# Performance work log

Measured on AMD Instinct MI355X. Metric: run time of the kernel, lower is better.

The kernel has to match this reference:

```python
import jax, jax.numpy as jnp
import numpy as np

B, S, D, H, T = 16, 512, 512, 8, 8
DK = D // H
SCALE = float(1.0 / np.sqrt(DK))
EPS = 1e-5


def setup_inputs() -> dict:
    key = jax.random.key(0)
    ks = jax.random.split(key, 12)
    s = float(1.0 / np.sqrt(D))  # torch Linear default init scale
    u = lambda k, shp: jax.random.uniform(k, shp, jnp.float32, -s, s)
    return {
        "x": jax.random.normal(ks[0], (B, S, D), jnp.float32),
        "x_type": jax.random.randint(ks[1], (B, S), 0, T, jnp.int32),
        "mask": jax.random.randint(ks[2], (B, S, S), 0, 2, jnp.int32),
        "Wq": u(ks[3], (T, D, D)), "bq": u(ks[4], (T, D)),
        "Wk": u(ks[5], (T, D, D)), "bk": u(ks[6], (T, D)),
        "Wv": u(ks[7], (T, D, D)), "bv": u(ks[8], (T, D)),
        "Wa": u(ks[9], (T, D, D)), "ba": u(ks[10], (T, D)),
        "gamma": jnp.ones((T, D), jnp.float32),
        "beta": jnp.zeros((T, D), jnp.float32),
    }


def _typed_proj(xf, t, W, b):
    # per-node-type linear 'experts': compute all T projections, select by type id
    # xf: [N, D], W: [T, D, D], b: [T, D], t: [N] -> [N, D]
    all_p = jnp.einsum('nd,tdh->nth', xf, W) + b[None]  # [N, T, D]
    return jnp.take_along_axis(all_p, t[:, None, None], axis=1)[:, 0]


def reference(x, x_type, mask, Wq, bq, Wk, bk, Wv, bv, Wa, ba, gamma, beta):
    xf = x.reshape(-1, D)          # [N, D], N = B*S
    t = x_type.reshape(-1)         # [N]

    # heterogeneous Q/K/V dispatch
    q = _typed_proj(xf, t, Wq, bq).reshape(B, S, H, DK).transpose(0, 2, 1, 3)
    k = _typed_proj(xf, t, Wk, bk).reshape(B, S, H, DK).transpose(0, 2, 1, 3)
    v = _typed_proj(xf, t, Wv, bv).reshape(B, S, H, DK).transpose(0, 2, 1, 3)

    # scaled dot-product attention with boolean mask (mask==0 -> -1e9)
    scores = jnp.einsum('bhqd,bhkd->bhqk', q, k) * SCALE  # [B, H, S, S]
    scores = jnp.where(mask[:, None] == 0, jnp.float32(-1e9), scores)
    p = jax.nn.softmax(scores, axis=-1)
    att = jnp.einsum('bhqk,bhkd->bhqd', p, v)             # [B, H, S, DK]
    att = att.transpose(0, 2, 1, 3).reshape(-1, D)        # [N, D]

    # per-type output projection + residual + per-type LayerNorm
    a = _typed_proj(att, t, Wa, ba)
    h = a + xf
    mu = jnp.mean(h, axis=-1, keepdims=True)
    var = jnp.mean((h - mu) ** 2, axis=-1, keepdims=True)
    out = (h - mu) * jax.lax.rsqrt(var + EPS) * gamma[t] + beta[t]
    return out.reshape(B, S, D)
```

## Files before the change

kernel.cpp:

```cpp
#include <hip/hip_runtime.h>
#include <hip/hip_bf16.h>

typedef __attribute__((ext_vector_type(8))) short short8;
typedef __attribute__((ext_vector_type(4))) float f32x4;
typedef __attribute__((ext_vector_type(4))) unsigned short u16x4;
typedef unsigned short u16;
typedef unsigned int u32;
typedef unsigned long long u64;

#define NB 16
#define NS 512
#define ND 512
#define NH 8
#define NT 8
#define NDK 64
#define NN (NB*NS)
#define SCALE_LOG2E 0.18033688011112042f
#define BM 128
#define BN 128
#define BKK 64

__device__ __forceinline__ u16 f2bf(float f) {
    __hip_bfloat16 h = __float2bfloat16(f);
    return *reinterpret_cast<u16*>(&h);
}
__device__ __forceinline__ float bf2f(u16 b) {
    u32 u = ((u32)b) << 16;
    return *reinterpret_cast<float*>(&u);
}
__device__ __forceinline__ u32 pk2(float lo, float hi) {
    return (u32)f2bf(lo) | ((u32)f2bf(hi) << 16);
}

typedef const __attribute__((address_space(1))) void* gas_t;
typedef __attribute__((address_space(3))) void* las_t;

__device__ __forceinline__ void gload16(const void* gsrc, void* ldst) {
    __builtin_amdgcn_global_load_lds((gas_t)gsrc, (las_t)ldst, 16, 0, 0);
}

__global__ __launch_bounds__(256) void pre_all(
    const float* __restrict__ x, const int* __restrict__ xty, const int* __restrict__ mask,
    const float* __restrict__ Wq, const float* __restrict__ Wk,
    const float* __restrict__ Wv, const float* __restrict__ Wa,
    u16* __restrict__ xb,
    u16* __restrict__ Wqt, u16* __restrict__ Wkt, u16* __restrict__ Wvt, u16* __restrict__ Wat,
    u64* __restrict__ maskb, int* __restrict__ scnt)
{
    __shared__ __align__(16) float tile[64][68];
    __shared__ int cnt[NT];
    int bid = blockIdx.x, tid = threadIdx.x;

    if (bid < 4096) {
        int i = bid * 256 + tid;
        float4 v = reinterpret_cast<const float4*>(x)[i];
        u16x4 o;
        o.x = f2bf(v.x); o.y = f2bf(v.y); o.z = f2bf(v.z); o.w = f2bf(v.w);
        reinterpret_cast<u16x4*>(xb)[i] = o;
    } else if (bid < 6144) {
        int wid = bid - 4096;
        int bx = wid & 7, by = (wid >> 3) & 7, bz = wid >> 6;
        int arr = bz >> 3, t = bz & 7;
        const float* W = (arr == 0 ? Wq : arr == 1 ? Wk : arr == 2 ? Wv : Wa) + ((size_t)t << 18);
        u16* O = (arr == 0 ? Wqt : arr == 1 ? Wkt : arr == 2 ? Wvt : Wat) + ((size_t)t << 18);
        int d0 = bx * 64, h0 = by * 64;
        int tx = tid & 15, ty = tid >> 4;
        #pragma unroll
        for (int i = 0; i < 4; ++i) {
            int r = ty + i * 16;
            float4 v = *reinterpret_cast<const float4*>(&W[(size_t)(d0 + r) * ND + h0 + tx * 4]);
            *reinterpret_cast<float4*>(&tile[r][tx * 4]) = v;
        }
        __syncthreads();
        #pragma unroll
        for (int i = 0; i < 4; ++i) {
            int r = ty + i * 16;
            u16x4 o;
            o.x = f2bf(tile[tx * 4 + 0][r]);
            o.y = f2bf(tile[tx * 4 + 1][r]);
            o.z = f2bf(tile[tx * 4 + 2][r]);
            o.w = f2bf(tile[tx * 4 + 3][r]);
            *reinterpret_cast<u16x4*>(&O[(size_t)(h0 + r) * ND + d0 + tx * 4]) = o;
        }
    } else if (bid < 7168) {
        int base = (bid - 6144) * 16;
        #pragma unroll
        for (int c = 0; c < 16; ++c) {
            int i = (base + c) * 256 + tid;
            int v = mask[i];
            u64 bal = __ballot(v != 0);
            if ((tid & 63) == 0) maskb[i >> 6] = bal;
        }
    } else {
        int s = bid - 7168;
        if (tid < NT) cnt[tid] = 0;
        __syncthreads();
        if (tid < 128) atomicAdd(&cnt[xty[s * 128 + tid]], 1);
        __syncthreads();
        if (tid < NT) scnt[s * 8 + tid] = cnt[tid];
    }
}

__global__ __launch_bounds__(256) void scatter_k(
    const int* __restrict__ xty, const int* __restrict__ scnt,
    int* __restrict__ perm, int* __restrict__ typeoff,
    int* __restrict__ tile_type, int* __restrict__ tile_row0, int* __restrict__ ntiles)
{
    __shared__ int base[NT], tot[NT];
    int s = blockIdx.x, tid = threadIdx.x;
    if (tid < NT) {
        int tt = 0;
        for (int ss = 0; ss < 64; ++ss) tt += scnt[ss * 8 + tid];
        tot[tid] = tt;
    }
    __syncthreads();
    if (tid < NT) {
        int off = 0;
        for (int u = 0; u < tid; ++u) off += tot[u];
        base[tid] = off;
    }
    __syncthreads();
    {
        int t = tid & 7;
        for (int ss = tid >> 3; ss < s; ss += 32) atomicAdd(&base[t], scnt[ss * 8 + t]);
    }
    __syncthreads();
    if (tid < 128) {
        int n = s * 128 + tid;
        int t = xty[n];
        int p = atomicAdd(&base[t], 1);
        perm[p] = n;
    }
    if (s == 0 && tid == 0) {
        int acc = 0, nt = 0;
        for (int t = 0; t < NT; ++t) {
            typeoff[t] = acc;
            int c = tot[t];
            for (int r = 0; r < c; r += BM) { tile_type[nt] = t; tile_row0[nt] = acc + r; ++nt; }
            acc += c;
        }
        typeoff[NT] = acc;
        *ntiles = nt;
    }
}

__global__ __launch_bounds__(256) void qkv_gemm(
    const u16* __restrict__ xb,
    const u16* __restrict__ Wqt, const u16* __restrict__ Wkt, const u16* __restrict__ Wvt,
    const float* __restrict__ bq, const float* __restrict__ bk, const float* __restrict__ bv,
    const int* __restrict__ perm, const int* __restrict__ typeoff,
    const int* __restrict__ tile_type, const int* __restrict__ tile_row0, const int* __restrict__ ntiles,
    u16* __restrict__ qb, u16* __restrict__ kbf, u16* __restrict__ vb)
{
    int p = (blockIdx.x & 7) * 54 + (blockIdx.x >> 3);
    int tile = p / 6;
    if (tile >= *ntiles) return;
    int pairc = p % 6;
    int proj = pairc >> 1;
    int colbase = (pairc & 1) * 256;
    int t = tile_type[tile];
    int row0 = tile_row0[tile];
    int rows = typeoff[t + 1] - row0; if (rows > BM) rows = BM;
    const u16* W = (proj == 0 ? Wqt : proj == 1 ? Wkt : Wvt) + ((size_t)t << 18);
    const float* bias = (proj == 0 ? bq : proj == 1 ? bk : bv) + (t << 9);
    u16* outp = proj == 0 ? qb : proj == 1 ? kbf : vb;
    float qscale = proj == 0 ? SCALE_LOG2E : 1.f;

    __shared__ __align__(16) u16 smem[2][2][BM][BKK];
    __shared__ int stok[BM];

    int tid = threadIdx.x;
    if (tid < BM) stok[tid] = perm[row0 + (tid < rows ? tid : 0)];
    __syncthreads();

    int lane = tid & 63, w = tid >> 6;
    int wr = w >> 1, wc = w & 1;
    int fr = lane & 15, g = lane >> 4;
    int lrow = lane >> 3;
    int schunk = (lane & 7) ^ lrow;
    int tokA[4];
    #pragma unroll
    for (int k = 0; k < 4; ++k) tokA[k] = stok[w * 32 + k * 8 + lrow];

    auto stage = [&](int buf, int k0, int c0) {
        #pragma unroll
        for (int k = 0; k < 4; ++k) {
            gload16(xb + (((size_t)tokA[k]) << 9) + k0 + schunk * 8, &smem[buf][0][w * 32 + k * 8][0]);
            gload16(W + (((size_t)(c0 + w * 32 + k * 8 + lrow)) << 9) + k0 + schunk * 8,
                    &smem[buf][1][w * 32 + k * 8][0]);
        }
    };

    f32x4 acc[4][4] = {};

    auto epilogue = [&](int buf, int c0) {
        u16* sT = &smem[buf][0][0][0];
        #pragma unroll
        for (int n = 0; n < 4; ++n) {
            int wcol = wc * 64 + n * 16 + fr;
            float bv_ = bias[c0 + wcol];
            #pragma unroll
            for (int m = 0; m < 4; ++m)
                #pragma unroll
                for (int i = 0; i < 4; ++i) {
                    int r = wr * 64 + m * 16 + g * 4 + i;
                    int ch = (wcol >> 3) ^ (r & 7);
                    sT[r * 128 + ch * 8 + (wcol & 7)] = f2bf((acc[m][n][i] + bv_) * qscale);
                }
        }
        asm volatile("s_waitcnt lgkmcnt(0)" ::: "memory");
        __builtin_amdgcn_s_barrier();
        int r = tid >> 1, h2 = tid & 1;
        if (r < rows) {
            int tok = stok[r], b = tok >> 9, s = tok & 511;
            int h = (c0 >> 6) + h2;
            u16* dst = outp + ((size_t)((b * NH + h) * NS + s) << 6);
            #pragma unroll
            for (int j2 = 0; j2 < 8; ++j2) {
                int ch = (h2 * 8 + j2) ^ (r & 7);
                *reinterpret_cast<short8*>(dst + j2 * 8) =
                    *reinterpret_cast<const short8*>(&sT[r * 128 + ch * 8]);
            }
        }
        asm volatile("s_waitcnt lgkmcnt(0)" ::: "memory");
        __builtin_amdgcn_s_barrier();
        #pragma unroll
        for (int m = 0; m < 4; ++m)
            #pragma unroll
            for (int n = 0; n < 4; ++n)
                acc[m][n] = (f32x4){0.f, 0.f, 0.f, 0.f};
    };

    stage(0, 0, colbase);
    #pragma unroll
    for (int j = 0; j < 16; ++j) {
        int cur = j & 1;
        if (j < 15) {
            int jn = j + 1;
            stage(cur ^ 1, (jn & 7) * BKK, colbase + (jn >> 3) * BN);
            asm volatile("s_waitcnt vmcnt(8)" ::: "memory");
        } else {
            asm volatile("s_waitcnt vmcnt(0)" ::: "memory");
        }
        __builtin_amdgcn_s_barrier();

        const char* Ab = (const char*)&smem[cur][0][0][0];
        const char* Bb = (const char*)&smem[cur][1][0][0];
        #pragma unroll
        for (int ks = 0; ks < 2; ++ks) {
            short8 af[4], bfr[4];
            #pragma unroll
            for (int m = 0; m < 4; ++m) {
                int r = wr * 64 + m * 16 + fr;
                af[m] = *reinterpret_cast<const short8*>(Ab + r * 128 + (((ks * 4 + g) ^ (r & 7)) << 4));
            }
            #pragma unroll
            for (int n = 0; n < 4; ++n) {
                int r = wc * 64 + n * 16 + fr;
                bfr[n] = *reinterpret_cast<const short8*>(Bb + r * 128 + (((ks * 4 + g) ^ (r & 7)) << 4));
            }
            #pragma unroll
            for (int m = 0; m < 4; ++m)
                #pragma unroll
                for (int n = 0; n < 4; ++n)
                    acc[m][n] = __builtin_amdgcn_mfma_f32_16x16x32_bf16(af[m], bfr[n], acc[m][n], 0, 0, 0);
        }
        asm volatile("s_waitcnt lgkmcnt(0)" ::: "memory");
        __builtin_amdgcn_s_barrier();

        if (j == 7) epilogue(1, colbase);
    }
    epilogue(1, colbase + BN);
}

__global__ __launch_bounds__(256) void transp_v(const u16* __restrict__ vb, u16* __restrict__ vtb)
{
    int bh = blockIdx.y, s0 = blockIdx.x * 64;
    __shared__ __align__(16) u16 t[64][72];
    int tid = threadIdx.x;
    const u16* src = vb + ((size_t)bh << 15) + ((size_t)s0 << 6);
    #pragma unroll
    for (int it = 0; it < 2; ++it) {
        int idx = it * 256 + tid;
        int s = idx & 63, c = idx >> 6;
        short8 v = *reinterpret_cast<const short8*>(src + ((size_t)s << 6) + c * 8);
        #pragma unroll
        for (int j = 0; j < 8; ++j) t[c * 8 + j][s] = ((const u16*)&v)[j];
    }
    __syncthreads();
    u16* dst = vtb + ((size_t)bh << 15) + s0;
    #pragma unroll
    for (int it = 0; it < 2; ++it) {
        int idx = it * 256 + tid;
        int dk = idx >> 3, c = idx & 7;
        short8 v = *reinterpret_cast<const short8*>(&t[dk][c * 8]);
        *reinterpret_cast<short8*>(dst + (size_t)dk * NS + c * 8) = v;
    }
}

__global__ __launch_bounds__(256) void attn_mfma(
    const u16* __restrict__ qb, const u16* __restrict__ kbf, const u16* __restrict__ vtb,
    const u64* __restrict__ maskb, u16* __restrict__ attb)
{
    int work = (blockIdx.x & 7) * 128 + (blockIdx.x >> 3);
    int bh = work >> 3, jq = work & 7;
    int b = bh >> 3, h = bh & 7;
    int q0 = jq * 64;
    int tid = threadIdx.x, lane = tid & 63, w = tid >> 6;
    int ln15 = lane & 15, g = lane >> 4;

    __shared__ __align__(16) u16 sK[64 * 64];
    __shared__ __align__(16) u16 sVt[64 * 64];
    __shared__ __align__(16) u16 sP[4 * 16 * 68];

    const u16* Qg = qb + ((size_t)(bh * NS + q0 + w * 16 + ln15) << 6);
    short8 aq0 = *reinterpret_cast<const short8*>(Qg + g * 8);
    short8 aq1 = *reinterpret_cast<const short8*>(Qg + 32 + g * 8);

    const u16* Kg = kbf + ((size_t)bh << 15);
    const u16* Vtg = vtb + ((size_t)bh << 15);
    int srow = tid >> 3, schunk = tid & 7;

    const u64* Mq = maskb + ((size_t)((b << 9) + q0 + w * 16 + ln15)) * 8;
    float mrun = -3.0e38f, lrun = 0.f;
    f32x4 acc_o[4] = {};

    short8 kpre0 = *reinterpret_cast<const short8*>(Kg + ((size_t)srow << 6) + schunk * 8);
    short8 kpre1 = *reinterpret_cast<const short8*>(Kg + ((size_t)(srow + 32) << 6) + schunk * 8);
    short8 vpre0 = *reinterpret_cast<const short8*>(Vtg + (size_t)srow * NS + schunk * 8);
    short8 vpre1 = *reinterpret_cast<const short8*>(Vtg + (size_t)(srow + 32) * NS + schunk * 8);

    char* sPw = (char*)sP + w * 16 * 136;

    for (int j = 0; j < 8; ++j) {
        __syncthreads();
        {
            int r2 = srow + 32;
            *reinterpret_cast<short8*>((char*)sK  + srow * 128 + ((schunk * 16) ^ ((srow & 7) << 4))) = kpre0;
            *reinterpret_cast<short8*>((char*)sK  + r2   * 128 + ((schunk * 16) ^ ((r2   & 7) << 4))) = kpre1;
            *reinterpret_cast<short8*>((char*)sVt + srow * 128 + ((schunk * 16) ^ ((srow & 7) << 4))) = vpre0;
            *reinterpret_cast<short8*>((char*)sVt + r2   * 128 + ((schunk * 16) ^ ((r2   & 7) << 4))) = vpre1;
        }
        if (j < 7) {
            int j1 = j + 1;
            kpre0 = *reinterpret_cast<const short8*>(Kg + ((size_t)(j1 * 64 + srow) << 6) + schunk * 8);
            kpre1 = *reinterpret_cast<const short8*>(Kg + ((size_t)(j1 * 64 + srow + 32) << 6) + schunk * 8);
            vpre0 = *reinterpret_cast<const short8*>(Vtg + (size_t)srow * NS + j1 * 64 + schunk * 8);
            vpre1 = *reinterpret_cast<const short8*>(Vtg + (size_t)(srow + 32) * NS + j1 * 64 + schunk * 8);
        }
        __syncthreads();

        f32x4 accs[4] = {};
        __builtin_amdgcn_s_setprio(1);
        #pragma unroll
        for (int ks = 0; ks < 2; ++ks) {
            short8 bq_ = ks ? aq1 : aq0;
            #pragma unroll
            for (int n = 0; n < 4; ++n) {
                int row = n * 16 + ln15;
                short8 kfrag = *reinterpret_cast<const short8*>(
                    (char*)sK + row * 128 + (((ks * 64) + g * 16) ^ ((row & 7) << 4)));
                accs[n] = __builtin_amdgcn_mfma_f32_16x16x32_bf16(kfrag, bq_, accs[n], 0, 0, 0);
            }
        }
        __builtin_amdgcn_s_setprio(0);

        u64 mw = Mq[j];
        float sv[4][4];
        float mx = -3.0e38f;
        #pragma unroll
        for (int n = 0; n < 4; ++n) {
            u32 b4 = (u32)(mw >> (n * 16 + g * 4)) & 15u;
            #pragma unroll
            for (int r = 0; r < 4; ++r) {
                float s = (b4 >> r) & 1u ? accs[n][r] : -1.0e9f;
                sv[n][r] = s;
                mx = fmaxf(mx, s);
            }
        }
        mx = fmaxf(mx, __shfl_xor(mx, 16));
        mx = fmaxf(mx, __shfl_xor(mx, 32));

        if (__any(mx > mrun + 8.f)) {
            float nm = fmaxf(mrun, mx);
            float sc = exp2f(mrun - nm);
            mrun = nm;
            lrun *= sc;
            #pragma unroll
            for (int i = 0; i < 4; ++i) {
                float si = __shfl(sc, g * 4 + i);
                #pragma unroll
                for (int n2 = 0; n2 < 4; ++n2) acc_o[n2][i] *= si;
            }
        }

        float ps = 0.f;
        #pragma unroll
        for (int n = 0; n < 4; ++n) {
            float p0 = exp2f(sv[n][0] - mrun), p1 = exp2f(sv[n][1] - mrun);
            float p2 = exp2f(sv[n][2] - mrun), p3 = exp2f(sv[n][3] - mrun);
            ps += (p0 + p1) + (p2 + p3);
            *reinterpret_cast<u32*>(sPw + ln15 * 136 + n * 32 + g * 8 + 0) = pk2(p0, p1);
            *reinterpret_cast<u32*>(sPw + ln15 * 136 + n * 32 + g * 8 + 4) = pk2(p2, p3);
        }
        ps += __shfl_xor(ps, 16);
        ps += __shfl_xor(ps, 32);
        lrun += ps;

        __builtin_amdgcn_s_setprio(1);
        #pragma unroll
        for (int ks = 0; ks < 2; ++ks) {
            short8 ap = *reinterpret_cast<const short8*>(sPw + ln15 * 136 + ks * 64 + g * 16);
            #pragma unroll
            for (int n2 = 0; n2 < 4; ++n2) {
                int row = n2 * 16 + ln15;
                short8 vfrag = *reinterpret_cast<const short8*>(
                    (char*)sVt + row * 128 + (((ks * 64) + g * 16) ^ ((row & 7) << 4)));
                acc_o[n2] = __builtin_amdgcn_mfma_f32_16x16x32_bf16(ap, vfrag, acc_o[n2], 0, 0, 0);
            }
        }
        __builtin_amdgcn_s_setprio(0);
    }

    float linv = 1.f / lrun;
    #pragma unroll
    for (int i = 0; i < 4; ++i) {
        float li = __shfl(linv, g * 4 + i);
        int q = q0 + w * 16 + g * 4 + i;
        #pragma unroll
        for (int n2 = 0; n2 < 4; ++n2) {
            attb[((size_t)((b << 9) + q) << 9) + (h << 6) + n2 * 16 + ln15] =
                f2bf(acc_o[n2][i] * li);
        }
    }
}

__global__ __launch_bounds__(256) void out_gemm(
    const u16* __restrict__ attb, const u16* __restrict__ Wat, const float* __restrict__ ba,
    const int* __restrict__ perm, const int* __restrict__ typeoff,
    const int* __restrict__ tile_type, const int* __restrict__ tile_row0, const int* __restrict__ ntiles,
    const u16* __restrict__ xb, u16* __restrict__ hbuf)
{
    int work = (blockIdx.x & 7) * 36 + (blockIdx.x >> 3);
    int tile = work >> 2;
    if (tile >= *ntiles) return;
    int t = tile_type[tile];
    int row0 = tile_row0[tile];
    int rows = typeoff[t + 1] - row0; if (rows > BM) rows = BM;
    int col0 = (work & 3) * BN;
    const u16* W = Wat + ((size_t)t << 18);
    const float* bias = ba + (t << 9);

    __shared__ __align__(16) u16 As[2][BM][BKK];
    __shared__ __align__(16) u16 Bs[2][BM][BKK];
    __shared__ int stok[BM];

    int tid = threadIdx.x;
    if (tid < BM) stok[tid] = perm[row0 + (tid < rows ? tid : 0)];
    __syncthreads();

    int lane = tid & 63, w = tid >> 6;
    int wr = w >> 1, wc = w & 1;
    int fr = lane & 15, g = lane >> 4;

    int lrow = lane >> 3;
    int schunk = (lane & 7) ^ lrow;
    int tokA[4];
    #pragma unroll
    for (int k = 0; k < 4; ++k) tokA[k] = stok[w * 32 + k * 8 + lrow];

    auto stage = [&](int buf, int k0) {
        #pragma unroll
        for (int k = 0; k < 4; ++k) {
            gload16(attb + (((size_t)tokA[k]) << 9) + k0 + schunk * 8, &As[buf][w * 32 + k * 8][0]);
            gload16(W + (((size_t)(col0 + w * 32 + k * 8 + lrow)) << 9) + k0 + schunk * 8,
                    &Bs[buf][w * 32 + k * 8][0]);
        }
    };

    f32x4 acc[4][4] = {};

    stage(0, 0);
    #pragma unroll
    for (int it = 0; it < 8; ++it) {
        int cur = it & 1;
        if (it < 7) {
            stage(cur ^ 1, (it + 1) * BKK);
            asm volatile("s_waitcnt vmcnt(8)" ::: "memory");
        } else {
            asm volatile("s_waitcnt vmcnt(0)" ::: "memory");
        }
        __builtin_amdgcn_s_barrier();

        const char* Ab = (const char*)As[cur];
        const char* Bb = (const char*)Bs[cur];
        #pragma unroll
        for (int ks = 0; ks < 2; ++ks) {
            short8 af[4], bfr[4];
            #pragma unroll
            for (int m = 0; m < 4; ++m) {
                int r = wr * 64 + m * 16 + fr;
                af[m] = *reinterpret_cast<const short8*>(Ab + r * 128 + (((ks * 4 + g) ^ (r & 7)) << 4));
            }
            #pragma unroll
            for (int n = 0; n < 4; ++n) {
                int r = wc * 64 + n * 16 + fr;
                bfr[n] = *reinterpret_cast<const short8*>(Bb + r * 128 + (((ks * 4 + g) ^ (r & 7)) << 4));
            }
            #pragma unroll
            for (int m = 0; m < 4; ++m)
                #pragma unroll
                for (int n = 0; n < 4; ++n)
                    acc[m][n] = __builtin_amdgcn_mfma_f32_16x16x32_bf16(af[m], bfr[n], acc[m][n], 0, 0, 0);
        }
        asm volatile("s_waitcnt lgkmcnt(0)" ::: "memory");
        __builtin_amdgcn_s_barrier();
    }

    int rbase = g << 2;
    #pragma unroll
    for (int n = 0; n < 4; ++n) {
        int c = col0 + wc * 64 + n * 16 + fr;
        float bv_ = bias[c];
        #pragma unroll
        for (int m = 0; m < 4; ++m) {
            #pragma unroll
            for (int i = 0; i < 4; ++i) {
                int r = wr * 64 + m * 16 + rbase + i;
                if (r < rows) {
                    int tok = stok[r];
                    size_t off = (size_t)tok * ND + c;
                    hbuf[off] = f2bf(acc[m][n][i] + bv_ + bf2f(xb[off]));
                }
            }
        }
    }
}

__global__ __launch_bounds__(256) void lnorm(
    const u16* __restrict__ hbuf, const int* __restrict__ xty,
    const float* __restrict__ gamma, const float* __restrict__ beta, float* __restrict__ out)
{
    int row = blockIdx.x * 4 + (threadIdx.x >> 6);
    int lane = threadIdx.x & 63;
    short8 v = *reinterpret_cast<const short8*>(hbuf + (size_t)row * ND + lane * 8);
    float f[8];
    float sum = 0.f, sq = 0.f;
    #pragma unroll
    for (int k = 0; k < 8; ++k) {
        f[k] = bf2f(((const u16*)&v)[k]);
        sum += f[k];
        sq += f[k] * f[k];
    }
    #pragma unroll
    for (int off = 32; off; off >>= 1) { sum += __shfl_xor(sum, off); sq += __shfl_xor(sq, off); }
    float mu = sum * (1.f / ND);
    float var = sq * (1.f / ND) - mu * mu;
    float is = rsqrtf(var + 1e-5f);
    int t = xty[row];
    const float4* g4 = reinterpret_cast<const float4*>(gamma + ((size_t)t << 9) + lane * 8);
    const float4* b4 = reinterpret_cast<const float4*>(beta + ((size_t)t << 9) + lane * 8);
    float4 g0 = g4[0], g1 = g4[1];
    float4 b0 = b4[0], b1 = b4[1];
    float4 o0, o1;
    o0.x = (f[0] - mu) * is * g0.x + b0.x;
    o0.y = (f[1] - mu) * is * g0.y + b0.y;
    o0.z = (f[2] - mu) * is * g0.z + b0.z;
    o0.w = (f[3] - mu) * is * g0.w + b0.w;
    o1.x = (f[4] - mu) * is * g1.x + b1.x;
    o1.y = (f[5] - mu) * is * g1.y + b1.y;
    o1.z = (f[6] - mu) * is * g1.z + b1.z;
    o1.w = (f[7] - mu) * is * g1.w + b1.w;
    float4* out4 = reinterpret_cast<float4*>(out + (size_t)row * ND + lane * 8);
    out4[0] = o0; out4[1] = o1;
}

extern "C" void kernel_launch(void* const* d_in, const int* in_sizes, int n_in,
                              void* d_out, int out_size, void* d_ws, size_t ws_size,
                              hipStream_t stream)
{
    const float* x     = (const float*)d_in[0];
    const int*   xty   = (const int*)d_in[1];
    const int*   mask  = (const int*)d_in[2];
    const float* Wq    = (const float*)d_in[3];
    const float* bq    = (const float*)d_in[4];
    const float* Wk    = (const float*)d_in[5];
    const float* bk    = (const float*)d_in[6];
    const float* Wv    = (const float*)d_in[7];
    const float* bv    = (const float*)d_in[8];
    const float* Wa    = (const float*)d_in[9];
    const float* ba    = (const float*)d_in[10];
    const float* gamma = (const float*)d_in[11];
    const float* beta  = (const float*)d_in[12];
    float* out = (float*)d_out;

    char* ws = (char*)d_ws;
    u16*   xb      = (u16*)(ws + 0);
    u16*   Wqt     = (u16*)(ws + 8388608);
    u16*   Wkt     = (u16*)(ws + 12582912);
    u16*   Wvt     = (u16*)(ws + 16777216);
    u16*   Wat     = (u16*)(ws + 20971520);
    u16*   qb      = (u16*)(ws + 25165824);
    u16*   kbf     = (u16*)(ws + 33554432);
    u16*   vb      = (u16*)(ws + 41943040);
    u16*   vtb     = (u16*)(ws + 50331648);
    u16*   attb    = (u16*)(ws + 58720256);
    u16*   hbuf    = (u16*)(ws + 67108864);
    u64*   maskb   = (u64*)(ws + 83886080);
    int*   perm    = (int*)(ws + 84410368);
    int*   typeoff = (int*)(ws + 84443136);
    int*   ttile   = (int*)(ws + 84443200);
    int*   trow    = (int*)(ws + 84443776);
    int*   ntiles  = (int*)(ws + 84444352);
    int*   scnt    = (int*)(ws + 84444480);

    pre_all<<<dim3(7232), dim3(256), 0, stream>>>(x, xty, mask, Wq, Wk, Wv, Wa,
                                                  xb, Wqt, Wkt, Wvt, Wat, maskb, scnt);
    scatter_k<<<dim3(64), dim3(256), 0, stream>>>(xty, scnt, perm, typeoff, ttile, trow, ntiles);
    qkv_gemm<<<dim3(432), dim3(256), 0, stream>>>(xb, Wqt, Wkt, Wvt, bq, bk, bv,
                                                  perm, typeoff, ttile, trow, ntiles, qb, kbf, vb);
    transp_v<<<dim3(8, 128), dim3(256), 0, stream>>>(vb, vtb);
    attn_mfma<<<dim3(1024), dim3(256), 0, stream>>>(qb, kbf, vtb, maskb, attb);
    out_gemm<<<dim3(288), dim3(256), 0, stream>>>(attb, Wat, ba,
                                                  perm, typeoff, ttile, trow, ntiles, xb, hbuf);
    lnorm<<<dim3(2048), dim3(256), 0, stream>>>(hbuf, xty, gamma, beta, out);
}
```

Measured before the change: 251.2 us.

## Split QKV GEMM to one column tile per block and keep P in registers

The QKV GEMM now assigns one 128-column tile per block instead of two, which doubles the grid and removes the mid-loop epilogue. The epilogue uses a padded unswizzled staging array. In attention, the softmax probabilities are packed straight into MFMA operand registers instead of going through a shared-memory sP buffer. The V tile stores into LDS are permuted with 4-element writes to match that register layout. The change trades the A-tile reuse across column tiles for more parallelism, and it relies on the new V permutation matching the implicit P fragment order.

```diff
diff --git a/kernel.cpp b/kernel.cpp
--- a/kernel.cpp
+++ b/kernel.cpp
@@ -152,15 +152,14 @@
     const int* __restrict__ tile_type, const int* __restrict__ tile_row0, const int* __restrict__ ntiles,
     u16* __restrict__ qb, u16* __restrict__ kbf, u16* __restrict__ vb)
 {
-    int p = (blockIdx.x & 7) * 54 + (blockIdx.x >> 3);
-    int tile = p / 6;
+    int work = (blockIdx.x & 7) * 108 + (blockIdx.x >> 3);
+    int tile = work / 12, pc = work % 12;
     if (tile >= *ntiles) return;
-    int pairc = p % 6;
-    int proj = pairc >> 1;
-    int colbase = (pairc & 1) * 256;
     int t = tile_type[tile];
     int row0 = tile_row0[tile];
     int rows = typeoff[t + 1] - row0; if (rows > BM) rows = BM;
+    int proj = pc >> 2;
+    int col0 = (pc & 3) * BN;
     const u16* W = (proj == 0 ? Wqt : proj == 1 ? Wkt : Wvt) + ((size_t)t << 18);
     const float* bias = (proj == 0 ? bq : proj == 1 ? bk : bv) + (t << 9);
     u16* outp = proj == 0 ? qb : proj == 1 ? kbf : vb;
@@ -168,6 +167,7 @@
 
     __shared__ __align__(16) u16 smem[2][2][BM][BKK];
     __shared__ int stok[BM];
+    auto As = smem[0]; auto Bs = smem[1];
 
     int tid = threadIdx.x;
     if (tid < BM) stok[tid] = perm[row0 + (tid < rows ? tid : 0)];
@@ -176,76 +176,38 @@
     int lane = tid & 63, w = tid >> 6;
     int wr = w >> 1, wc = w & 1;
     int fr = lane & 15, g = lane >> 4;
+
     int lrow = lane >> 3;
     int schunk = (lane & 7) ^ lrow;
     int tokA[4];
     #pragma unroll
     for (int k = 0; k < 4; ++k) tokA[k] = stok[w * 32 + k * 8 + lrow];
 
-    auto stage = [&](int buf, int k0, int c0) {
+    auto stage = [&](int buf, int k0) {
         #pragma unroll
         for (int k = 0; k < 4; ++k) {
-            gload16(xb + (((size_t)tokA[k]) << 9) + k0 + schunk * 8, &smem[buf][0][w * 32 + k * 8][0]);
-            gload16(W + (((size_t)(c0 + w * 32 + k * 8 + lrow)) << 9) + k0 + schunk * 8,
-                    &smem[buf][1][w * 32 + k * 8][0]);
+            gload16(xb + (((size_t)tokA[k]) << 9) + k0 + schunk * 8, &As[buf][w * 32 + k * 8][0]);
+            gload16(W + (((size_t)(col0 + w * 32 + k * 8 + lrow)) << 9) + k0 + schunk * 8,
+                    &Bs[buf][w * 32 + k * 8][0]);
         }
     };
 
     f32x4 acc[4][4] = {};
 
-    auto epilogue = [&](int buf, int c0) {
-        u16* sT = &smem[buf][0][0][0];
-        #pragma unroll
-        for (int n = 0; n < 4; ++n) {
-            int wcol = wc * 64 + n * 16 + fr;
-            float bv_ = bias[c0 + wcol];
-            #pragma unroll
-            for (int m = 0; m < 4; ++m)
-                #pragma unroll
-                for (int i = 0; i < 4; ++i) {
-                    int r = wr * 64 + m * 16 + g * 4 + i;
-                    int ch = (wcol >> 3) ^ (r & 7);
-                    sT[r * 128 + ch * 8 + (wcol & 7)] = f2bf((acc[m][n][i] + bv_) * qscale);
-                }
-        }
-        asm volatile("s_waitcnt lgkmcnt(0)" ::: "memory");
-        __builtin_amdgcn_s_barrier();
-        int r = tid >> 1, h2 = tid & 1;
-        if (r < rows) {
-            int tok = stok[r], b = tok >> 9, s = tok & 511;
-            int h = (c0 >> 6) + h2;
-            u16* dst = outp + ((size_t)((b * NH + h) * NS + s) << 6);
-            #pragma unroll
-            for (int j2 = 0; j2 < 8; ++j2) {
-                int ch = (h2 * 8 + j2) ^ (r & 7);
-                *reinterpret_cast<short8*>(dst + j2 * 8) =
-                    *reinterpret_cast<const short8*>(&sT[r * 128 + ch * 8]);
-            }
-        }
-        asm volatile("s_waitcnt lgkmcnt(0)" ::: "memory");
-        __builtin_amdgcn_s_barrier();
-        #pragma unroll
-        for (int m = 0; m < 4; ++m)
-            #pragma unroll
-            for (int n = 0; n < 4; ++n)
-                acc[m][n] = (f32x4){0.f, 0.f, 0.f, 0.f};
-    };
-
-    stage(0, 0, colbase);
-    #pragma unroll
-    for (int j = 0; j < 16; ++j) {
-        int cur = j & 1;
-        if (j < 15) {
-            int jn = j + 1;
-            stage(cur ^ 1, (jn & 7) * BKK, colbase + (jn >> 3) * BN);
+    stage(0, 0);
+    #pragma unroll
+    for (int it = 0; it < 8; ++it) {
+        int cur = it & 1;
+        if (it < 7) {
+            stage(cur ^ 1, (it + 1) * BKK);
             asm volatile("s_waitcnt vmcnt(8)" ::: "memory");
         } else {
             asm volatile("s_waitcnt vmcnt(0)" ::: "memory");
         }
         __builtin_amdgcn_s_barrier();
 
-        const char* Ab = (const char*)&smem[cur][0][0][0];
-        const char* Bb = (const char*)&smem[cur][1][0][0];
+        const char* Ab = (const char*)As[cur];
+        const char* Bb = (const char*)Bs[cur];
         #pragma unroll
         for (int ks = 0; ks < 2; ++ks) {
             short8 af[4], bfr[4];
@@ -267,10 +229,30 @@
         }
         asm volatile("s_waitcnt lgkmcnt(0)" ::: "memory");
         __builtin_amdgcn_s_barrier();
-
-        if (j == 7) epilogue(1, colbase);
-    }
-    epilogue(1, colbase + BN);
+    }
+
+    u16 (*sT)[136] = reinterpret_cast<u16 (*)[136]>(&smem[0][0][0][0]);
+    #pragma unroll
+    for (int n = 0; n < 4; ++n) {
+        int col = wc * 64 + n * 16 + fr;
+        float bv_ = bias[col0 + col];
+        #pragma unroll
+        for (int m = 0; m < 4; ++m)
+            #pragma unroll
+            for (int i = 0; i < 4; ++i)
+                sT[wr * 64 + m * 16 + g * 4 + i][col] = f2bf((acc[m][n][i] + bv_) * qscale);
+    }
+    __syncthreads();
+    int r = tid >> 1, half = tid & 1;
+    if (r < rows) {
+        int tok = stok[r], b = tok >> 9, s = tok & 511;
+        int h = (col0 >> 6) + half;
+        u16* dst = outp + ((size_t)((b * NH + h) * NS + s) << 6);
+        #pragma unroll
+        for (int j = 0; j < 8; ++j)
+            *reinterpret_cast<short8*>(dst + j * 8) =
+                *reinterpret_cast<const short8*>(&sT[r][half * 64 + j * 8]);
+    }
 }
 
 __global__ __launch_bounds__(256) void transp_v(const u16* __restrict__ vb, u16* __restrict__ vtb)
@@ -311,7 +293,6 @@
 
     __shared__ __align__(16) u16 sK[64 * 64];
     __shared__ __align__(16) u16 sVt[64 * 64];
-    __shared__ __align__(16) u16 sP[4 * 16 * 68];
 
     const u16* Qg = qb + ((size_t)(bh * NS + q0 + w * 16 + ln15) << 6);
     short8 aq0 = *reinterpret_cast<const short8*>(Qg + g * 8);
@@ -320,6 +301,10 @@
     const u16* Kg = kbf + ((size_t)bh << 15);
     const u16* Vtg = vtb + ((size_t)bh << 15);
     int srow = tid >> 3, schunk = tid & 7;
+
+    int vks = schunk >> 2, vhalf = (schunk >> 1) & 1, vg0 = (schunk & 1) * 2;
+    int vchunk0 = vks * 4 + vg0;
+    int vchunk1 = vchunk0 + 1;
 
     const u64* Mq = maskb + ((size_t)((b << 9) + q0 + w * 16 + ln15)) * 8;
     float mrun = -3.0e38f, lrun = 0.f;
@@ -330,16 +315,20 @@
     short8 vpre0 = *reinterpret_cast<const short8*>(Vtg + (size_t)srow * NS + schunk * 8);
     short8 vpre1 = *reinterpret_cast<const short8*>(Vtg + (size_t)(srow + 32) * NS + schunk * 8);
 
-    char* sPw = (char*)sP + w * 16 * 136;
-
     for (int j = 0; j < 8; ++j) {
         __syncthreads();
         {
             int r2 = srow + 32;
-            *reinterpret_cast<short8*>((char*)sK  + srow * 128 + ((schunk * 16) ^ ((srow & 7) << 4))) = kpre0;
-            *reinterpret_cast<short8*>((char*)sK  + r2   * 128 + ((schunk * 16) ^ ((r2   & 7) << 4))) = kpre1;
-            *reinterpret_cast<short8*>((char*)sVt + srow * 128 + ((schunk * 16) ^ ((srow & 7) << 4))) = vpre0;
-            *reinterpret_cast<short8*>((char*)sVt + r2   * 128 + ((schunk * 16) ^ ((r2   & 7) << 4))) = vpre1;
+            *reinterpret_cast<short8*>((char*)sK + srow * 128 + ((schunk * 16) ^ ((srow & 7) << 4))) = kpre0;
+            *reinterpret_cast<short8*>((char*)sK + r2   * 128 + ((schunk * 16) ^ ((r2   & 7) << 4))) = kpre1;
+            u16x4 vlo0 = { (u16)vpre0[0], (u16)vpre0[1], (u16)vpre0[2], (u16)vpre0[3] };
+            u16x4 vhi0 = { (u16)vpre0[4], (u16)vpre0[5], (u16)vpre0[6], (u16)vpre0[7] };
+            u16x4 vlo1 = { (u16)vpre1[0], (u16)vpre1[1], (u16)vpre1[2], (u16)vpre1[3] };
+            u16x4 vhi1 = { (u16)vpre1[4], (u16)vpre1[5], (u16)vpre1[6], (u16)vpre1[7] };
+            *reinterpret_cast<u16x4*>((char*)sVt + srow * 128 + (((vchunk0) ^ (srow & 7)) << 4) + vhalf * 8) = vlo0;
+            *reinterpret_cast<u16x4*>((char*)sVt + srow * 128 + (((vchunk1) ^ (srow & 7)) << 4) + vhalf * 8) = vhi0;
+            *reinterpret_cast<u16x4*>((char*)sVt + r2 * 128 + (((vchunk0) ^ (r2 & 7)) << 4) + vhalf * 8) = vlo1;
+            *reinterpret_cast<u16x4*>((char*)sVt + r2 * 128 + (((vchunk1) ^ (r2 & 7)) << 4) + vhalf * 8) = vhi1;
         }
         if (j < 7) {
             int j1 = j + 1;
@@ -394,14 +383,15 @@
             }
         }
 
+        float p[4][4];
         float ps = 0.f;
         #pragma unroll
         for (int n = 0; n < 4; ++n) {
-            float p0 = exp2f(sv[n][0] - mrun), p1 = exp2f(sv[n][1] - mrun);
-            float p2 = exp2f(sv[n][2] - mrun), p3 = exp2f(sv[n][3] - mrun);
-            ps += (p0 + p1) + (p2 + p3);
-            *reinterpret_cast<u32*>(sPw + ln15 * 136 + n * 32 + g * 8 + 0) = pk2(p0, p1);
-            *reinterpret_cast<u32*>(sPw + ln15 * 136 + n * 32 + g * 8 + 4) = pk2(p2, p3);
+            #pragma unroll
+            for (int r = 0; r < 4; ++r) {
+                p[n][r] = exp2f(sv[n][r] - mrun);
+                ps += p[n][r];
+            }
         }
         ps += __shfl_xor(ps, 16);
         ps += __shfl_xor(ps, 32);
@@ -410,7 +400,12 @@
         __builtin_amdgcn_s_setprio(1);
         #pragma unroll
         for (int ks = 0; ks < 2; ++ks) {
-            short8 ap = *reinterpret_cast<const short8*>(sPw + ln15 * 136 + ks * 64 + g * 16);
+            short8 ap;
+            u32* apw = reinterpret_cast<u32*>(&ap);
+            apw[0] = pk2(p[ks * 2][0], p[ks * 2][1]);
+            apw[1] = pk2(p[ks * 2][2], p[ks * 2][3]);
+            apw[2] = pk2(p[ks * 2 + 1][0], p[ks * 2 + 1][1]);
+            apw[3] = pk2(p[ks * 2 + 1][2], p[ks * 2 + 1][3]);
             #pragma unroll
             for (int n2 = 0; n2 < 4; ++n2) {
                 int row = n2 * 16 + ln15;
@@ -617,7 +612,7 @@
     pre_all<<<dim3(7232), dim3(256), 0, stream>>>(x, xty, mask, Wq, Wk, Wv, Wa,
                                                   xb, Wqt, Wkt, Wvt, Wat, maskb, scnt);
     scatter_k<<<dim3(64), dim3(256), 0, stream>>>(xty, scnt, perm, typeoff, ttile, trow, ntiles);
-    qkv_gemm<<<dim3(432), dim3(256), 0, stream>>>(xb, Wqt, Wkt, Wvt, bq, bk, bv,
+    qkv_gemm<<<dim3(864), dim3(256), 0, stream>>>(xb, Wqt, Wkt, Wvt, bq, bk, bv,
                                                   perm, typeoff, ttile, trow, ntiles, qb, kbf, vb);
     transp_v<<<dim3(8, 128), dim3(256), 0, stream>>>(vb, vtb);
     attn_mfma<<<dim3(1024), dim3(256), 0, stream>>>(qb, kbf, vtb, maskb, attb);
```

Result: no change. 248.1 us (-1.2%).
